# Kernel optimization log

Measured on AMD Instinct MI355X. Metric: run time of the kernel, lower is better.

Reference implementation:

```python
import jax, jax.numpy as jnp
import numpy as np

B, L, D_IN, D_H, D_OUT = 8, 1024, 1024, 1024, 1024


def setup_inputs() -> dict:
    key = jax.random.key(0)
    ks = jax.random.split(key, 9)
    s = 0.02  # weight scale to keep ReLU chain stable
    return {
        "leaves": jax.random.normal(ks[0], (B, L, D_IN), dtype=jnp.float32),
        "V_w": jax.random.normal(ks[1], (D_H, D_IN), dtype=jnp.float32) * s,
        "V_b": jax.random.normal(ks[2], (D_H,), dtype=jnp.float32) * s,
        "U_w": jax.random.normal(ks[3], (D_H, D_H), dtype=jnp.float32) * s,
        "U_b": jax.random.normal(ks[4], (D_H,), dtype=jnp.float32) * s,
        "W_w": jax.random.normal(ks[5], (D_H, D_H), dtype=jnp.float32) * s,
        "W_b": jax.random.normal(ks[6], (D_H,), dtype=jnp.float32) * s,
        "O_w": jax.random.normal(ks[7], (D_OUT, D_H), dtype=jnp.float32) * s,
        "O_b": jax.random.normal(ks[8], (D_OUT,), dtype=jnp.float32) * s,
    }


def reference(leaves, V_w, V_b, U_w, U_b, W_w, W_b, O_w, O_b):
    # Leaf encoding: h_leaf = relu(V(x))            [B, L, H]
    h = jax.nn.relu(jnp.einsum("bli,hi->blh", leaves, V_w) + V_b)
    # Depth-batched recursion over the complete binary tree:
    # combined = relu(U(left) + W(right)); log2(L) levels, node count halves.
    while h.shape[1] > 1:
        left, right = h[:, 0::2], h[:, 1::2]  # [B, n/2, H] each
        h = jax.nn.relu(
            jnp.einsum("bnh,gh->bng", left, U_w) + U_b
            + jnp.einsum("bnh,gh->bng", right, W_w) + W_b
        )
    root = h[:, 0]  # [B, H]
    logits = jnp.einsum("bh,oh->bo", root, O_w) + O_b
    return jax.nn.log_softmax(logits, axis=-1)
```

## Files before the change

kernel.cpp:

```cpp
#include <hip/hip_runtime.h>
#include <hip/hip_bf16.h>
#include <math.h>

typedef __bf16 bf16_t;
typedef __bf16 bf16x8 __attribute__((ext_vector_type(8)));
typedef __bf16 bf16x4 __attribute__((ext_vector_type(4)));
typedef float  f32x4  __attribute__((ext_vector_type(4)));

#define GLD_LDS16(g, l)                                                          \
  __builtin_amdgcn_global_load_lds((const __attribute__((address_space(1))) void*)(g), \
                                   (__attribute__((address_space(3))) void*)(l), 16, 0, 0)

__global__ __launch_bounds__(256) void k_cvt_all(const float* __restrict__ leaves,
                                                 const float* __restrict__ V_w,
                                                 const float* __restrict__ O_w,
                                                 const float* __restrict__ U_w,
                                                 const float* __restrict__ W_w,
                                                 const float* __restrict__ U_b,
                                                 const float* __restrict__ W_b,
                                                 bf16_t* __restrict__ leaves_bf,
                                                 bf16_t* __restrict__ Vw_bf,
                                                 bf16_t* __restrict__ Ow_bf,
                                                 bf16_t* __restrict__ UW_bf,
                                                 float* __restrict__ buw) {
  const int gtid = blockIdx.x * 256 + threadIdx.x;
  const int G = gridDim.x * 256;
  for (int i = gtid; i < 2097152; i += G) {
    float4 v = reinterpret_cast<const float4*>(leaves)[i];
    bf16x4 o; o[0] = (bf16_t)v.x; o[1] = (bf16_t)v.y; o[2] = (bf16_t)v.z; o[3] = (bf16_t)v.w;
    reinterpret_cast<bf16x4*>(leaves_bf)[i] = o;
  }
  for (int i = gtid; i < 262144; i += G) {
    float4 v = reinterpret_cast<const float4*>(V_w)[i];
    bf16x4 o; o[0] = (bf16_t)v.x; o[1] = (bf16_t)v.y; o[2] = (bf16_t)v.z; o[3] = (bf16_t)v.w;
    reinterpret_cast<bf16x4*>(Vw_bf)[i] = o;
  }
  for (int i = gtid; i < 262144; i += G) {
    float4 v = reinterpret_cast<const float4*>(O_w)[i];
    bf16x4 o; o[0] = (bf16_t)v.x; o[1] = (bf16_t)v.y; o[2] = (bf16_t)v.z; o[3] = (bf16_t)v.w;
    reinterpret_cast<bf16x4*>(Ow_bf)[i] = o;
  }
  for (int idx = gtid; idx < 524288; idx += G) {
    int i = idx * 4;
    int g = i >> 11;
    int k = i & 2047;
    const float* src = (k < 1024) ? (U_w + g * 1024 + k) : (W_w + g * 1024 + (k - 1024));
    float4 v = *reinterpret_cast<const float4*>(src);
    bf16x4 o; o[0] = (bf16_t)v.x; o[1] = (bf16_t)v.y; o[2] = (bf16_t)v.z; o[3] = (bf16_t)v.w;
    reinterpret_cast<bf16x4*>(UW_bf)[idx] = o;
  }
  if (gtid < 1024) buw[gtid] = U_b[gtid] + W_b[gtid];
}

template <int TM, int TN, bool SPLIT>
__global__ __launch_bounds__(256, (TM == 128 ? 2 : 3)) void k_gemm(
    const bf16_t* __restrict__ A, const bf16_t* __restrict__ Bw,
    const float* __restrict__ bias, bf16_t* __restrict__ C,
    bf16_t* __restrict__ P, int M, int Kstride, int kchunk) {
  constexpr int MI = TM / 32;
  constexpr int NJ = TN / 32;
  constexpr int VM = TM / 64 + TN / 64;
  __shared__ bf16_t As[4][TM * 32];
  __shared__ bf16_t Bs[4][TN * 32];

  const int tid = threadIdx.x;
  const int lane = tid & 63;
  const int wave = tid >> 6;
  const int wr = wave >> 1, wc = wave & 1;
  const int bm = blockIdx.x, bn = blockIdx.y, bz = blockIdx.z;

  const bf16_t* Abase = A + (size_t)bm * TM * Kstride + (size_t)bz * kchunk;
  const bf16_t* Bbase = Bw + (size_t)bn * TN * Kstride + (size_t)bz * kchunk;

  f32x4 acc[MI][NJ] = {};
  const int rl = lane & 15, kq = lane >> 4;

  auto stage = [&](int buf, int ko) {
#pragma unroll
    for (int it = 0; it < TM / 64; ++it) {
      int c = tid + 256 * it;
      int r = c >> 2, kbp = c & 3;
      int kb = kbp ^ ((r >> 1) & 3);
      GLD_LDS16(Abase + (size_t)r * Kstride + ko + kb * 8, &As[buf][c * 8]);
    }
#pragma unroll
    for (int it = 0; it < TN / 64; ++it) {
      int c = tid + 256 * it;
      int r = c >> 2, kbp = c & 3;
      int kb = kbp ^ ((r >> 1) & 3);
      GLD_LDS16(Bbase + (size_t)r * Kstride + ko + kb * 8, &Bs[buf][c * 8]);
    }
  };

  const int kiters = kchunk >> 5;
  stage(0, 0);
  if (kiters > 1) stage(1, 32);
  if (kiters > 2) stage(2, 64);

  int cur = 0;
  for (int t = 0; t < kiters; ++t) {
    const int nin = kiters - 1 - t;
    if (nin >= 2)      asm volatile("s_waitcnt vmcnt(%0)" :: "i"(2 * VM) : "memory");
    else if (nin == 1) asm volatile("s_waitcnt vmcnt(%0)" :: "i"(VM) : "memory");
    else               asm volatile("s_waitcnt vmcnt(0)" ::: "memory");
    __builtin_amdgcn_s_barrier();
    __builtin_amdgcn_sched_barrier(0);
    if (t + 3 < kiters) {
      int b3 = cur + 3; if (b3 >= 4) b3 -= 4;
      stage(b3, (t + 3) * 32);
    }
    bf16x8 af[MI], bfr[NJ];
#pragma unroll
    for (int i = 0; i < MI; ++i) {
      int r = wr * (TM / 2) + i * 16 + rl;
      int kbp = kq ^ ((r >> 1) & 3);
      af[i] = *reinterpret_cast<const bf16x8*>(&As[cur][r * 32 + kbp * 8]);
    }
#pragma unroll
    for (int j = 0; j < NJ; ++j) {
      int r = wc * (TN / 2) + j * 16 + rl;
      int kbp = kq ^ ((r >> 1) & 3);
      bfr[j] = *reinterpret_cast<const bf16x8*>(&Bs[cur][r * 32 + kbp * 8]);
    }
#pragma unroll
    for (int i = 0; i < MI; ++i)
#pragma unroll
      for (int j = 0; j < NJ; ++j)
        acc[i][j] = __builtin_amdgcn_mfma_f32_16x16x32_bf16(af[i], bfr[j], acc[i][j], 0, 0, 0);
    if (++cur >= 4) cur = 0;
  }

  const int rq = lane >> 4, cl = lane & 15;
  if (SPLIT) {
    bf16_t* Pp = P + (size_t)bz * M * 1024;
#pragma unroll
    for (int j = 0; j < NJ; ++j) {
      int gcol = bn * TN + wc * (TN / 2) + j * 16 + cl;
#pragma unroll
      for (int i = 0; i < MI; ++i) {
        int grow = bm * TM + wr * (TM / 2) + i * 16 + rq * 4;
#pragma unroll
        for (int reg = 0; reg < 4; ++reg)
          Pp[(size_t)(grow + reg) * 1024 + gcol] = (bf16_t)acc[i][j][reg];
      }
    }
  } else {
#pragma unroll
    for (int j = 0; j < NJ; ++j) {
      int gcol = bn * TN + wc * (TN / 2) + j * 16 + cl;
      float bv = bias[gcol];
#pragma unroll
      for (int i = 0; i < MI; ++i) {
        int grow = bm * TM + wr * (TM / 2) + i * 16 + rq * 4;
#pragma unroll
        for (int reg = 0; reg < 4; ++reg) {
          float v = acc[i][j][reg] + bv;
          v = v > 0.0f ? v : 0.0f;
          C[(size_t)(grow + reg) * 1024 + gcol] = (bf16_t)v;
        }
      }
    }
  }
}

__global__ __launch_bounds__(256) void k_reduce(const bf16_t* __restrict__ P,
                                                const float* __restrict__ bias,
                                                bf16_t* __restrict__ C, int M, int ks) {
  constexpr int N = 1024;
  int idx = blockIdx.x * 256 + threadIdx.x;
  int col = (idx * 4) & (N - 1);
  int row = (idx * 4) >> 10;
  float s0 = 0.0f, s1 = 0.0f, s2 = 0.0f, s3 = 0.0f;
  for (int z = 0; z < ks; ++z) {
    bf16x4 v = *reinterpret_cast<const bf16x4*>(P + ((size_t)z * M + row) * N + col);
    s0 += (float)v[0]; s1 += (float)v[1]; s2 += (float)v[2]; s3 += (float)v[3];
  }
  float4 b = *reinterpret_cast<const float4*>(bias + col);
  bf16x4 o;
  o[0] = (bf16_t)fmaxf(s0 + b.x, 0.0f);
  o[1] = (bf16_t)fmaxf(s1 + b.y, 0.0f);
  o[2] = (bf16_t)fmaxf(s2 + b.z, 0.0f);
  o[3] = (bf16_t)fmaxf(s3 + b.w, 0.0f);
  reinterpret_cast<bf16x4*>(C)[idx] = o;
}

template <int KK, bool RELU, bool F32OUT>
__global__ __launch_bounds__(256) void k_tail(const bf16_t* __restrict__ A,
                                              const bf16_t* __restrict__ Bw,
                                              const float* __restrict__ bias,
                                              void* __restrict__ Cout, int M) {
  constexpr int N = 1024;
  constexpr int KPL = KK / 64;
  const int lane = threadIdx.x & 63;
  const int gw = blockIdx.x * 4 + (threadIdx.x >> 6);
  const int n = gw & (N - 1);
  const int mbase = (gw >> 10) * 8;
  const int k0 = lane * KPL;

  float bv[KPL];
  const bf16_t* bp = Bw + (size_t)n * KK + k0;
#pragma unroll
  for (int q = 0; q < KPL / 8; ++q) {
    bf16x8 v = *reinterpret_cast<const bf16x8*>(bp + q * 8);
#pragma unroll
    for (int j = 0; j < 8; ++j) bv[q * 8 + j] = (float)v[j];
  }

  float acc[8];
#pragma unroll
  for (int m = 0; m < 8; ++m) {
    const bf16_t* ap = A + (size_t)(mbase + m) * KK + k0;
    float s = 0.0f;
#pragma unroll
    for (int q = 0; q < KPL / 8; ++q) {
      bf16x8 v = *reinterpret_cast<const bf16x8*>(ap + q * 8);
#pragma unroll
      for (int j = 0; j < 8; ++j) s += (float)v[j] * bv[q * 8 + j];
    }
    acc[m] = s;
  }
#pragma unroll
  for (int m = 0; m < 8; ++m) {
#pragma unroll
    for (int off = 32; off >= 1; off >>= 1) acc[m] += __shfl_xor(acc[m], off, 64);
  }
  if (lane < 8 && mbase + lane < M) {
    float v = acc[lane] + bias[n];
    if (RELU) v = v > 0.0f ? v : 0.0f;
    if (F32OUT) ((float*)Cout)[(size_t)(mbase + lane) * N + n] = v;
    else        ((bf16_t*)Cout)[(size_t)(mbase + lane) * N + n] = (bf16_t)v;
  }
}

__global__ __launch_bounds__(256) void k_logsoftmax(const float* __restrict__ logits,
                                                    float* __restrict__ out) {
  int b = blockIdx.x;
  const float* x = logits + b * 1024;
  int tid = threadIdx.x;
  int wave = tid >> 6, lane = tid & 63;
  __shared__ float red[8];

  float m = -1e30f;
  for (int i = tid; i < 1024; i += 256) m = fmaxf(m, x[i]);
#pragma unroll
  for (int off = 32; off >= 1; off >>= 1) m = fmaxf(m, __shfl_xor(m, off, 64));
  if (lane == 0) red[wave] = m;
  __syncthreads();
  m = fmaxf(fmaxf(red[0], red[1]), fmaxf(red[2], red[3]));
  float s = 0.0f;
  for (int i = tid; i < 1024; i += 256) s += expf(x[i] - m);
#pragma unroll
  for (int off = 32; off >= 1; off >>= 1) s += __shfl_xor(s, off, 64);
  if (lane == 0) red[wave] = s;
  __syncthreads();
  float lse = m + logf(red[0] + red[1] + red[2] + red[3]);
  for (int i = tid; i < 1024; i += 256) out[b * 1024 + i] = x[i] - lse;
}

extern "C" void kernel_launch(void* const* d_in, const int* in_sizes, int n_in,
                              void* d_out, int out_size, void* d_ws, size_t ws_size,
                              hipStream_t stream) {
  const float* leaves = (const float*)d_in[0];
  const float* V_w = (const float*)d_in[1];
  const float* V_b = (const float*)d_in[2];
  const float* U_w = (const float*)d_in[3];
  const float* U_b = (const float*)d_in[4];
  const float* W_w = (const float*)d_in[5];
  const float* W_b = (const float*)d_in[6];
  const float* O_w = (const float*)d_in[7];
  const float* O_b = (const float*)d_in[8];
  float* out = (float*)d_out;

  char* ws = (char*)d_ws;
  size_t off = 0;
  auto alloc = [&](size_t bytes) -> void* {
    off = (off + 255) & ~(size_t)255;
    void* p = ws + off;
    off += bytes;
    return p;
  };

  const size_t MB16 = (size_t)8192 * 1024 * 2;
  bf16_t* leaves_bf = (bf16_t*)alloc(MB16);
  bf16_t* Vw_bf = (bf16_t*)alloc((size_t)1024 * 1024 * 2);
  bf16_t* UW_bf = (bf16_t*)alloc((size_t)2 * 1024 * 1024 * 2);
  bf16_t* Ow_bf = (bf16_t*)alloc((size_t)1024 * 1024 * 2);
  float* buw = (float*)alloc(1024 * 4);
  bf16_t* hA = (bf16_t*)alloc(MB16);
  float* logits = (float*)alloc(8 * 1024 * 4);
  bf16_t* Pbuf = (bf16_t*)alloc((size_t)8 * 4096 * 1024 * 2);
  (void)ws_size; (void)in_sizes; (void)n_in; (void)out_size;

  k_cvt_all<<<2048, 256, 0, stream>>>(leaves, V_w, O_w, U_w, W_w, U_b, W_b,
                                      leaves_bf, Vw_bf, Ow_bf, UW_bf, buw);

  k_gemm<128, 128, false><<<dim3(64, 8), 256, 0, stream>>>(
      leaves_bf, Vw_bf, V_b, hA, nullptr, 8192, 1024, 1024);

  bf16_t* src = hA;
  bf16_t* dst = leaves_bf;
  auto swap = [&]() { bf16_t* t = src; src = dst; dst = t; };

  k_gemm<128, 128, true><<<dim3(32, 8, 2), 256, 0, stream>>>(
      src, UW_bf, nullptr, nullptr, Pbuf, 4096, 2048, 1024);
  k_reduce<<<4096 * 1024 / 4 / 256, 256, 0, stream>>>(Pbuf, buw, dst, 4096, 2);
  swap();
  k_gemm<64, 128, true><<<dim3(32, 8, 2), 256, 0, stream>>>(
      src, UW_bf, nullptr, nullptr, Pbuf, 2048, 2048, 1024);
  k_reduce<<<2048 * 1024 / 4 / 256, 256, 0, stream>>>(Pbuf, buw, dst, 2048, 2);
  swap();
  k_gemm<64, 128, true><<<dim3(16, 8, 4), 256, 0, stream>>>(
      src, UW_bf, nullptr, nullptr, Pbuf, 1024, 2048, 512);
  k_reduce<<<1024 * 1024 / 4 / 256, 256, 0, stream>>>(Pbuf, buw, dst, 1024, 4);
  swap();
  k_gemm<64, 128, true><<<dim3(8, 8, 4), 256, 0, stream>>>(
      src, UW_bf, nullptr, nullptr, Pbuf, 512, 2048, 512);
  k_reduce<<<512 * 1024 / 4 / 256, 256, 0, stream>>>(Pbuf, buw, dst, 512, 4);
  swap();
  k_gemm<64, 128, true><<<dim3(4, 8, 8), 256, 0, stream>>>(
      src, UW_bf, nullptr, nullptr, Pbuf, 256, 2048, 256);
  k_reduce<<<256 * 1024 / 4 / 256, 256, 0, stream>>>(Pbuf, buw, dst, 256, 8);
  swap();
  k_gemm<64, 128, true><<<dim3(2, 8, 8), 256, 0, stream>>>(
      src, UW_bf, nullptr, nullptr, Pbuf, 128, 2048, 256);
  k_reduce<<<128 * 1024 / 4 / 256, 256, 0, stream>>>(Pbuf, buw, dst, 128, 8);
  swap();
  for (int M = 64; M >= 8; M >>= 1) {
    int blocks = (M / 8) * 1024 / 4;
    k_tail<2048, true, false><<<blocks, 256, 0, stream>>>(src, UW_bf, buw, dst, M);
    swap();
  }

  k_tail<1024, false, true><<<256, 256, 0, stream>>>(src, Ow_bf, O_b, logits, 8);
  k_logsoftmax<<<8, 256, 0, stream>>>(logits, out);
}
```

Baseline: 207.0 us.

## Fuse split-K reduction into GEMM via last-arriving-block atomic counter

```diff
diff --git a/kernel.cpp b/kernel.cpp
--- a/kernel.cpp
+++ b/kernel.cpp
@@ -22,7 +22,8 @@
                                                  bf16_t* __restrict__ Vw_bf,
                                                  bf16_t* __restrict__ Ow_bf,
                                                  bf16_t* __restrict__ UW_bf,
-                                                 float* __restrict__ buw) {
+                                                 float* __restrict__ buw,
+                                                 int* __restrict__ flags) {
   const int gtid = blockIdx.x * 256 + threadIdx.x;
   const int G = gridDim.x * 256;
   for (int i = gtid; i < 2097152; i += G) {
@@ -50,13 +51,15 @@
     reinterpret_cast<bf16x4*>(UW_bf)[idx] = o;
   }
   if (gtid < 1024) buw[gtid] = U_b[gtid] + W_b[gtid];
+  if (gtid < 1536) flags[gtid] = 0;
 }
 
 template <int TM, int TN, bool SPLIT>
 __global__ __launch_bounds__(256, (TM == 128 ? 2 : 3)) void k_gemm(
     const bf16_t* __restrict__ A, const bf16_t* __restrict__ Bw,
     const float* __restrict__ bias, bf16_t* __restrict__ C,
-    bf16_t* __restrict__ P, int M, int Kstride, int kchunk) {
+    bf16_t* __restrict__ P, int* __restrict__ flag,
+    int M, int Kstride, int kchunk) {
   constexpr int MI = TM / 32;
   constexpr int NJ = TN / 32;
   constexpr int VM = TM / 64 + TN / 64;
@@ -144,6 +147,37 @@
           Pp[(size_t)(grow + reg) * 1024 + gcol] = (bf16_t)acc[i][j][reg];
       }
     }
+    asm volatile("s_waitcnt vmcnt(0)" ::: "memory");
+    __syncthreads();
+    __shared__ int sh_fin;
+    if (tid == 0) {
+      int* f = &flag[bm * 8 + bn];
+      int old = __hip_atomic_fetch_add(f, 1, __ATOMIC_RELEASE, __HIP_MEMORY_SCOPE_AGENT);
+      int fin = (old == (int)gridDim.z - 1);
+      if (fin)
+        (void)__hip_atomic_load(f, __ATOMIC_ACQUIRE, __HIP_MEMORY_SCOPE_AGENT);
+      sh_fin = fin;
+    }
+    __syncthreads();
+    if (sh_fin) {
+      const int ks = (int)gridDim.z;
+      for (int e = tid * 4; e < TM * TN; e += 1024) {
+        int rr = e / TN, cc = e % TN;
+        int grow = bm * TM + rr, gcol = bn * TN + cc;
+        float s0 = 0.f, s1 = 0.f, s2 = 0.f, s3 = 0.f;
+        for (int z = 0; z < ks; ++z) {
+          bf16x4 v = *reinterpret_cast<const bf16x4*>(P + ((size_t)z * M + grow) * 1024 + gcol);
+          s0 += (float)v[0]; s1 += (float)v[1]; s2 += (float)v[2]; s3 += (float)v[3];
+        }
+        float4 b = *reinterpret_cast<const float4*>(bias + gcol);
+        bf16x4 o;
+        o[0] = (bf16_t)fmaxf(s0 + b.x, 0.0f);
+        o[1] = (bf16_t)fmaxf(s1 + b.y, 0.0f);
+        o[2] = (bf16_t)fmaxf(s2 + b.z, 0.0f);
+        o[3] = (bf16_t)fmaxf(s3 + b.w, 0.0f);
+        *reinterpret_cast<bf16x4*>(C + (size_t)grow * 1024 + gcol) = o;
+      }
+    }
   } else {
 #pragma unroll
     for (int j = 0; j < NJ; ++j) {
@@ -161,27 +195,6 @@
       }
     }
   }
-}
-
-__global__ __launch_bounds__(256) void k_reduce(const bf16_t* __restrict__ P,
-                                                const float* __restrict__ bias,
-                                                bf16_t* __restrict__ C, int M, int ks) {
-  constexpr int N = 1024;
-  int idx = blockIdx.x * 256 + threadIdx.x;
-  int col = (idx * 4) & (N - 1);
-  int row = (idx * 4) >> 10;
-  float s0 = 0.0f, s1 = 0.0f, s2 = 0.0f, s3 = 0.0f;
-  for (int z = 0; z < ks; ++z) {
-    bf16x4 v = *reinterpret_cast<const bf16x4*>(P + ((size_t)z * M + row) * N + col);
-    s0 += (float)v[0]; s1 += (float)v[1]; s2 += (float)v[2]; s3 += (float)v[3];
-  }
-  float4 b = *reinterpret_cast<const float4*>(bias + col);
-  bf16x4 o;
-  o[0] = (bf16_t)fmaxf(s0 + b.x, 0.0f);
-  o[1] = (bf16_t)fmaxf(s1 + b.y, 0.0f);
-  o[2] = (bf16_t)fmaxf(s2 + b.z, 0.0f);
-  o[3] = (bf16_t)fmaxf(s3 + b.w, 0.0f);
-  reinterpret_cast<bf16x4*>(C)[idx] = o;
 }
 
 template <int KK, bool RELU, bool F32OUT>
@@ -289,41 +302,36 @@
   bf16_t* hA = (bf16_t*)alloc(MB16);
   float* logits = (float*)alloc(8 * 1024 * 4);
   bf16_t* Pbuf = (bf16_t*)alloc((size_t)8 * 4096 * 1024 * 2);
+  int* flags = (int*)alloc(1536 * 4);
   (void)ws_size; (void)in_sizes; (void)n_in; (void)out_size;
 
   k_cvt_all<<<2048, 256, 0, stream>>>(leaves, V_w, O_w, U_w, W_w, U_b, W_b,
-                                      leaves_bf, Vw_bf, Ow_bf, UW_bf, buw);
+                                      leaves_bf, Vw_bf, Ow_bf, UW_bf, buw, flags);
 
   k_gemm<128, 128, false><<<dim3(64, 8), 256, 0, stream>>>(
-      leaves_bf, Vw_bf, V_b, hA, nullptr, 8192, 1024, 1024);
+      leaves_bf, Vw_bf, V_b, hA, nullptr, nullptr, 8192, 1024, 1024);
 
   bf16_t* src = hA;
   bf16_t* dst = leaves_bf;
   auto swap = [&]() { bf16_t* t = src; src = dst; dst = t; };
 
   k_gemm<128, 128, true><<<dim3(32, 8, 2), 256, 0, stream>>>(
-      src, UW_bf, nullptr, nullptr, Pbuf, 4096, 2048, 1024);
-  k_reduce<<<4096 * 1024 / 4 / 256, 256, 0, stream>>>(Pbuf, buw, dst, 4096, 2);
+      src, UW_bf, buw, dst, Pbuf, flags + 0 * 256, 4096, 2048, 1024);
   swap();
   k_gemm<64, 128, true><<<dim3(32, 8, 2), 256, 0, stream>>>(
-      src, UW_bf, nullptr, nullptr, Pbuf, 2048, 2048, 1024);
-  k_reduce<<<2048 * 1024 / 4 / 256, 256, 0, stream>>>(Pbuf, buw, dst, 2048, 2);
+      src, UW_bf, buw, dst, Pbuf, flags + 1 * 256, 2048, 2048, 1024);
   swap();
   k_gemm<64, 128, true><<<dim3(16, 8, 4), 256, 0, stream>>>(
-      src, UW_bf, nullptr, nullptr, Pbuf, 1024, 2048, 512);
-  k_reduce<<<1024 * 1024 / 4 / 256, 256, 0, stream>>>(Pbuf, buw, dst, 1024, 4);
+      src, UW_bf, buw, dst, Pbuf, flags + 2 * 256, 1024, 2048, 512);
   swap();
   k_gemm<64, 128, true><<<dim3(8, 8, 4), 256, 0, stream>>>(
-      src, UW_bf, nullptr, nullptr, Pbuf, 512, 2048, 512);
-  k_reduce<<<512 * 1024 / 4 / 256, 256, 0, stream>>>(Pbuf, buw, dst, 512, 4);
+      src, UW_bf, buw, dst, Pbuf, flags + 3 * 256, 512, 2048, 512);
   swap();
   k_gemm<64, 128, true><<<dim3(4, 8, 8), 256, 0, stream>>>(
-      src, UW_bf, nullptr, nullptr, Pbuf, 256, 2048, 256);
-  k_reduce<<<256 * 1024 / 4 / 256, 256, 0, stream>>>(Pbuf, buw, dst, 256, 8);
+      src, UW_bf, buw, dst, Pbuf, flags + 4 * 256, 256, 2048, 256);
   swap();
   k_gemm<64, 128, true><<<dim3(2, 8, 8), 256, 0, stream>>>(
-      src, UW_bf, nullptr, nullptr, Pbuf, 128, 2048, 256);
-  k_reduce<<<128 * 1024 / 4 / 256, 256, 0, stream>>>(Pbuf, buw, dst, 128, 8);
+      src, UW_bf, buw, dst, Pbuf, flags + 5 * 256, 128, 2048, 256);
   swap();
   for (int M = 64; M >= 8; M >>= 1) {
     int blocks = (M / 8) * 1024 / 4;
```

Measured after the change: 330.6 us. 59.7% more time.
